# Kernel optimization log

Measured on AMD Instinct MI355X. Metric: run time of the kernel, lower is better.

The kernel has to match this reference:

```python
import jax, jax.numpy as jnp
import numpy as np

EPS = 1e-6
TEMP = 1.0
L = 64  # shapelet_len


def _znorm(a):
    # z-normalize over last axis, population std, clamped by EPS (matches torch unbiased=False + clamp_min)
    mean = a.mean(axis=-1, keepdims=True)
    std = jnp.maximum(a.std(axis=-1, keepdims=True), EPS)
    return (a - mean) / std


def setup_inputs() -> dict:
    key = jax.random.key(0)
    k1, k2 = jax.random.split(key)
    bs, T, C, P = 32, 8192, 1, 64
    x = jax.random.normal(k1, (bs, T, C), dtype=jnp.float32)
    shapelets = jax.random.normal(k2, (P, C, L), dtype=jnp.float32)
    return {"x": x, "shapelets": shapelets}


def reference(x, shapelets):
    # x: [bs, T, C]; shapelets: [P, C, L]
    bs, T, C = x.shape
    P = shapelets.shape[0]
    x_ct = jnp.transpose(x, (0, 2, 1))  # [bs, C, T]
    Tp = T - L + 1
    # sliding windows: [bs, C, T', L]
    idx = jnp.arange(Tp)[:, None] + jnp.arange(L)[None, :]
    w = x_ct[:, :, idx]
    # z-normalize windows and shapelets over the length axis
    w = _znorm(w)
    s = _znorm(shapelets)
    # squared euclidean distance via expansion ||w||^2 - 2 w.s + ||s||^2 (sum over C and L)
    w2 = jnp.sum(w * w, axis=(1, 3))          # [bs, T']
    s2 = jnp.sum(s * s, axis=(1, 2))          # [P]
    dot = jnp.einsum('bctl,pcl->btp', w, s)   # [bs, T', P]
    dist2 = w2[:, :, None] + s2[None, None, :] - 2.0 * dot
    temp = max(TEMP, EPS)
    act = jnp.exp(-dist2 / temp)              # [bs, T', P]
    # center-pad to length T: left = L//2, right = T - (T' + left)
    left = L // 2
    right = max(0, T - (Tp + left))
    act_full = jnp.pad(act, ((0, 0), (left, right), (0, 0)))
    return act_full[:, :T, :]
```

## Files before the change

### kernel.cpp

```cpp
#include <hip/hip_runtime.h>
#include <math.h>

#define T_LEN 8192
#define EPSF  1e-6f

typedef __attribute__((ext_vector_type(8))) short short8;
typedef __attribute__((ext_vector_type(4))) float float4v;

__global__ __launch_bounds__(256, 4) void shapelet_fused(
        const float* __restrict__ x,
        const float* __restrict__ sh,
        float* __restrict__ out) {
    __shared__ float Sraw[64][65];
    __shared__ unsigned short Bhi[64][72];
    __shared__ unsigned short Blo[64][72];
    __shared__ float xs[192];
    __shared__ float lmu[128], linv[128], lw2[128];
    __shared__ float lsum[64], ls2[64];

    const int tid  = threadIdx.x;
    const int lane = tid & 63;
    const int wave = tid >> 6;
    const int n    = lane & 15;
    const int quad = lane >> 4;

    const int super = blockIdx.x & 63;
    const int b     = blockIdx.x >> 6;
    const int t0    = super << 7;

    {
        const float4* g4 = (const float4*)sh;
#pragma unroll
        for (int i = 0; i < 4; ++i) {
            int idx = tid + (i << 8);
            float4 v = g4[idx];
            int e = idx << 2;
            int row = e >> 6, col = e & 63;
            Sraw[row][col + 0] = v.x;
            Sraw[row][col + 1] = v.y;
            Sraw[row][col + 2] = v.z;
            Sraw[row][col + 3] = v.w;
        }
        if (tid < 192) {
            int g = t0 - 32 + tid;
            xs[tid] = ((unsigned)g < (unsigned)T_LEN) ? x[(size_t)b * T_LEN + g] : 0.f;
        }
    }
    __syncthreads();

    if (tid < 64) {
        const int p = tid;
        float s1 = 0.f;
        for (int l = 0; l < 64; ++l) s1 += Sraw[p][l];
        float mu = s1 * (1.f / 64.f);
        float sq = 0.f;
        for (int l = 0; l < 64; ++l) { float d = Sraw[p][l] - mu; sq = fmaf(d, d, sq); }
        float sd  = fmaxf(sqrtf(sq * (1.f / 64.f)), EPSF);
        float inv = 1.f / sd;
        float ssum = 0.f, ss2 = 0.f;
        for (int l2 = 0; l2 < 32; ++l2) {
            unsigned pk_h, pk_l;
            {
                float v = Sraw[p][2 * l2];
                float s = (v - mu) * inv;
                unsigned ub = __float_as_uint(s);
                float hi = __uint_as_float(ub & 0xFFFF0000u);
                float lo = s - hi;
                unsigned lb = __float_as_uint(lo) & 0xFFFF0000u;
                pk_h = ub >> 16;
                pk_l = lb >> 16;
                float eff = hi + __uint_as_float(lb);
                ssum += eff;
                ss2  = fmaf(eff, eff, ss2);
            }
            {
                float v = Sraw[p][2 * l2 + 1];
                float s = (v - mu) * inv;
                unsigned ub = __float_as_uint(s);
                float hi = __uint_as_float(ub & 0xFFFF0000u);
                float lo = s - hi;
                unsigned lb = __float_as_uint(lo) & 0xFFFF0000u;
                pk_h |= (ub & 0xFFFF0000u);
                pk_l |= lb;
                float eff = hi + __uint_as_float(lb);
                ssum += eff;
                ss2  = fmaf(eff, eff, ss2);
            }
            *(unsigned*)&Bhi[p][2 * l2] = pk_h;
            *(unsigned*)&Blo[p][2 * l2] = pk_l;
        }
        lsum[p] = ssum;
        ls2[p]  = ss2;
    } else if (tid < 192) {
        const int r = tid - 64;
        float s1 = 0.f, sq = 0.f;
#pragma unroll
        for (int l = 0; l < 64; ++l) {
            float v = xs[r + l];
            s1 += v; sq = fmaf(v, v, sq);
        }
        float mu  = s1 * (1.f / 64.f);
        float var = fmaxf(sq * (1.f / 64.f) - mu * mu, 0.f);
        float sd  = fmaxf(sqrtf(var), EPSF);
        float inv = 1.f / sd;
        lmu[r]  = mu;
        linv[r] = inv;
        lw2[r]  = 64.f * var * inv * inv;
    }
    __syncthreads();

    short8 Bh[4][2], Bl[4][2];
#pragma unroll
    for (int pt = 0; pt < 4; ++pt)
#pragma unroll
        for (int h = 0; h < 2; ++h) {
            Bh[pt][h] = *(const short8*)&Bhi[pt * 16 + n][h * 32 + (quad << 3)];
            Bl[pt][h] = *(const short8*)&Blo[pt * 16 + n][h * 32 + (quad << 3)];
        }

#pragma unroll
    for (int u = 0; u < 2; ++u) {
        const int abase = (u << 6) + (wave << 4) + n + (quad << 3);
        short8 Ah[2], Al[2];
#pragma unroll
        for (int h = 0; h < 2; ++h) {
#pragma unroll
            for (int j = 0; j < 8; ++j) {
                float v = xs[abase + h * 32 + j];
                unsigned ub = __float_as_uint(v);
                unsigned hb = ub & 0xFFFF0000u;
                float lo = v - __uint_as_float(hb);
                Ah[h][j] = (short)(ub >> 16);
                Al[h][j] = (short)(__float_as_uint(lo) >> 16);
            }
        }

        float4v acc[4];
#pragma unroll
        for (int pt = 0; pt < 4; ++pt) {
            float4v a = {0.f, 0.f, 0.f, 0.f};
#pragma unroll
            for (int h = 0; h < 2; ++h) {
                a = __builtin_amdgcn_mfma_f32_16x16x32_bf16(Ah[h], Bh[pt][h], a, 0, 0, 0);
                a = __builtin_amdgcn_mfma_f32_16x16x32_bf16(Ah[h], Bl[pt][h], a, 0, 0, 0);
                a = __builtin_amdgcn_mfma_f32_16x16x32_bf16(Al[h], Bh[pt][h], a, 0, 0, 0);
            }
            acc[pt] = a;
        }

        float sm[4], sv[4];
#pragma unroll
        for (int pt = 0; pt < 4; ++pt) { sm[pt] = lsum[pt * 16 + n]; sv[pt] = ls2[pt * 16 + n]; }
#pragma unroll
        for (int r = 0; r < 4; ++r) {
            int tl = (u << 6) + (wave << 4) + (quad << 2) + r;
            int tg = t0 + tl;
            bool valid = (tg >= 32) && (tg <= 8160);
            float mu  = lmu[tl];
            float inv = linv[tl];
            float w2  = lw2[tl];
            float* orow = out + ((size_t)(b * T_LEN + tg) << 6);
#pragma unroll
            for (int pt = 0; pt < 4; ++pt) {
                float dot  = (acc[pt][r] - mu * sm[pt]) * inv;
                float dist = w2 + sv[pt] - 2.f * dot;
                orow[pt * 16 + n] = valid ? __expf(-dist) : 0.f;
            }
        }
    }
}

extern "C" void kernel_launch(void* const* d_in, const int* in_sizes, int n_in,
                              void* d_out, int out_size, void* d_ws, size_t ws_size,
                              hipStream_t stream) {
    const float* x  = (const float*)d_in[0];
    const float* sh = (const float*)d_in[1];
    float* out = (float*)d_out;

    shapelet_fused<<<32 * 64, 256, 0, stream>>>(x, sh, out);
}
```

Measured before the change: 85.23 us.

## Permute shapelet columns and stage outputs through LDS for float4 stores

Shapelet rows are permuted so each lane's four MFMA output columns are contiguous, which allows lsum/ls2 to be read as float4 and results packed into float4. Each wave writes its 16x64 output tile into a per-wave LDS buffer that reuses the Sraw space through a union, then reads it back and issues coalesced 16-byte global stores instead of scattered 4-byte stores. The launch-bounds occupancy hint is lowered from 4 to 3 to give the compiler more registers. The cost is extra LDS traffic per tile.

```diff
diff --git a/kernel.cpp b/kernel.cpp
--- a/kernel.cpp
+++ b/kernel.cpp
@@ -7,16 +7,20 @@
 typedef __attribute__((ext_vector_type(8))) short short8;
 typedef __attribute__((ext_vector_type(4))) float float4v;
 
-__global__ __launch_bounds__(256, 4) void shapelet_fused(
+__global__ __launch_bounds__(256, 3) void shapelet_fused(
         const float* __restrict__ x,
         const float* __restrict__ sh,
         float* __restrict__ out) {
-    __shared__ float Sraw[64][65];
+    __shared__ union {
+        float Sraw[64][65];
+        float xpose[4][1024];
+    } S;
     __shared__ unsigned short Bhi[64][72];
     __shared__ unsigned short Blo[64][72];
     __shared__ float xs[192];
     __shared__ float lmu[128], linv[128], lw2[128];
-    __shared__ float lsum[64], ls2[64];
+    __shared__ __align__(16) float lsum[64];
+    __shared__ __align__(16) float ls2[64];
 
     const int tid  = threadIdx.x;
     const int lane = tid & 63;
@@ -36,10 +40,10 @@
             float4 v = g4[idx];
             int e = idx << 2;
             int row = e >> 6, col = e & 63;
-            Sraw[row][col + 0] = v.x;
-            Sraw[row][col + 1] = v.y;
-            Sraw[row][col + 2] = v.z;
-            Sraw[row][col + 3] = v.w;
+            S.Sraw[row][col + 0] = v.x;
+            S.Sraw[row][col + 1] = v.y;
+            S.Sraw[row][col + 2] = v.z;
+            S.Sraw[row][col + 3] = v.w;
         }
         if (tid < 192) {
             int g = t0 - 32 + tid;
@@ -50,18 +54,19 @@
 
     if (tid < 64) {
         const int p = tid;
+        const int c = ((p & 3) << 4) + (p >> 2);
         float s1 = 0.f;
-        for (int l = 0; l < 64; ++l) s1 += Sraw[p][l];
+        for (int l = 0; l < 64; ++l) s1 += S.Sraw[p][l];
         float mu = s1 * (1.f / 64.f);
         float sq = 0.f;
-        for (int l = 0; l < 64; ++l) { float d = Sraw[p][l] - mu; sq = fmaf(d, d, sq); }
+        for (int l = 0; l < 64; ++l) { float d = S.Sraw[p][l] - mu; sq = fmaf(d, d, sq); }
         float sd  = fmaxf(sqrtf(sq * (1.f / 64.f)), EPSF);
         float inv = 1.f / sd;
         float ssum = 0.f, ss2 = 0.f;
         for (int l2 = 0; l2 < 32; ++l2) {
             unsigned pk_h, pk_l;
             {
-                float v = Sraw[p][2 * l2];
+                float v = S.Sraw[p][2 * l2];
                 float s = (v - mu) * inv;
                 unsigned ub = __float_as_uint(s);
                 float hi = __uint_as_float(ub & 0xFFFF0000u);
@@ -74,7 +79,7 @@
                 ss2  = fmaf(eff, eff, ss2);
             }
             {
-                float v = Sraw[p][2 * l2 + 1];
+                float v = S.Sraw[p][2 * l2 + 1];
                 float s = (v - mu) * inv;
                 unsigned ub = __float_as_uint(s);
                 float hi = __uint_as_float(ub & 0xFFFF0000u);
@@ -86,8 +91,8 @@
                 ssum += eff;
                 ss2  = fmaf(eff, eff, ss2);
             }
-            *(unsigned*)&Bhi[p][2 * l2] = pk_h;
-            *(unsigned*)&Blo[p][2 * l2] = pk_l;
+            *(unsigned*)&Bhi[c][2 * l2] = pk_h;
+            *(unsigned*)&Blo[c][2 * l2] = pk_l;
         }
         lsum[p] = ssum;
         ls2[p]  = ss2;
@@ -117,6 +122,10 @@
             Bh[pt][h] = *(const short8*)&Bhi[pt * 16 + n][h * 32 + (quad << 3)];
             Bl[pt][h] = *(const short8*)&Blo[pt * 16 + n][h * 32 + (quad << 3)];
         }
+    const float4 sm4 = *(const float4*)&lsum[n << 2];
+    const float4 sv4 = *(const float4*)&ls2[n << 2];
+
+    float* tile = S.xpose[wave];
 
 #pragma unroll
     for (int u = 0; u < 2; ++u) {
@@ -148,24 +157,34 @@
             acc[pt] = a;
         }
 
-        float sm[4], sv[4];
-#pragma unroll
-        for (int pt = 0; pt < 4; ++pt) { sm[pt] = lsum[pt * 16 + n]; sv[pt] = ls2[pt * 16 + n]; }
 #pragma unroll
         for (int r = 0; r < 4; ++r) {
-            int tl = (u << 6) + (wave << 4) + (quad << 2) + r;
+            int rloc = (quad << 2) + r;
+            int tl = (u << 6) + (wave << 4) + rloc;
             int tg = t0 + tl;
             bool valid = (tg >= 32) && (tg <= 8160);
             float mu  = lmu[tl];
             float inv = linv[tl];
             float w2  = lw2[tl];
-            float* orow = out + ((size_t)(b * T_LEN + tg) << 6);
-#pragma unroll
-            for (int pt = 0; pt < 4; ++pt) {
-                float dot  = (acc[pt][r] - mu * sm[pt]) * inv;
-                float dist = w2 + sv[pt] - 2.f * dot;
-                orow[pt * 16 + n] = valid ? __expf(-dist) : 0.f;
-            }
+            float d0 = (acc[0][r] - mu * sm4.x) * inv;
+            float d1 = (acc[1][r] - mu * sm4.y) * inv;
+            float d2 = (acc[2][r] - mu * sm4.z) * inv;
+            float d3 = (acc[3][r] - mu * sm4.w) * inv;
+            float4 o;
+            o.x = valid ? __expf(-(w2 + sv4.x - 2.f * d0)) : 0.f;
+            o.y = valid ? __expf(-(w2 + sv4.y - 2.f * d1)) : 0.f;
+            o.z = valid ? __expf(-(w2 + sv4.z - 2.f * d2)) : 0.f;
+            o.w = valid ? __expf(-(w2 + sv4.w - 2.f * d3)) : 0.f;
+            *(float4*)&tile[(rloc << 6) + (n << 2)] = o;
+        }
+
+#pragma unroll
+        for (int s = 0; s < 4; ++s) {
+            float4 v = *(const float4*)&tile[(s << 8) + (lane << 2)];
+            int rloc = (s << 2) + (lane >> 4);
+            int tg = t0 + (u << 6) + (wave << 4) + rloc;
+            int col = (lane & 15) << 2;
+            *(float4*)(out + (((size_t)(b * T_LEN + tg)) << 6) + col) = v;
         }
     }
 }
```

Result: slower. 87.37 us (+2.5%).

## Permute shapelet columns for float4 output stores and double time-tile per block

Applied to the files above, without the earlier changes.

The shapelet rows are permuted in shared memory, so each lane's four MFMA output columns (one per tile) map to four consecutive shapelets. Each lane then writes a single float4 instead of four scalar stores. The block now covers 256 time steps instead of 128, which halves the grid and spreads the per-block shapelet normalization cost over more outputs. The x window is also loaded with float4. The trade-offs are less parallelism and more shared memory per block, and the window-statistics loop is now split unevenly across threads.

```diff
diff --git a/kernel.cpp b/kernel.cpp
--- a/kernel.cpp
+++ b/kernel.cpp
@@ -14,9 +14,10 @@
     __shared__ float Sraw[64][65];
     __shared__ unsigned short Bhi[64][72];
     __shared__ unsigned short Blo[64][72];
-    __shared__ float xs[192];
-    __shared__ float lmu[128], linv[128], lw2[128];
-    __shared__ float lsum[64], ls2[64];
+    __shared__ float xs[320];
+    __shared__ float lmu[256], linv[256], lw2[256];
+    __shared__ __align__(16) float lsum[64];
+    __shared__ __align__(16) float ls2[64];
 
     const int tid  = threadIdx.x;
     const int lane = tid & 63;
@@ -24,9 +25,9 @@
     const int n    = lane & 15;
     const int quad = lane >> 4;
 
-    const int super = blockIdx.x & 63;
-    const int b     = blockIdx.x >> 6;
-    const int t0    = super << 7;
+    const int super = blockIdx.x & 31;
+    const int b     = blockIdx.x >> 5;
+    const int t0    = super << 8;
 
     {
         const float4* g4 = (const float4*)sh;
@@ -41,15 +42,27 @@
             Sraw[row][col + 2] = v.z;
             Sraw[row][col + 3] = v.w;
         }
-        if (tid < 192) {
-            int g = t0 - 32 + tid;
-            xs[tid] = ((unsigned)g < (unsigned)T_LEN) ? x[(size_t)b * T_LEN + g] : 0.f;
+        if (tid < 80) {
+            int g0 = t0 - 32 + (tid << 2);
+            float4 v;
+            if (g0 >= 0 && g0 + 3 < T_LEN) {
+                v = *(const float4*)(x + (size_t)b * T_LEN + g0);
+            } else {
+                float* vp = (float*)&v;
+#pragma unroll
+                for (int e = 0; e < 4; ++e) {
+                    int g = g0 + e;
+                    vp[e] = ((unsigned)g < (unsigned)T_LEN) ? x[(size_t)b * T_LEN + g] : 0.f;
+                }
+            }
+            *(float4*)&xs[tid << 2] = v;
         }
     }
     __syncthreads();
 
     if (tid < 64) {
         const int p = tid;
+        const int c = ((p & 3) << 4) + (p >> 2);
         float s1 = 0.f;
         for (int l = 0; l < 64; ++l) s1 += Sraw[p][l];
         float mu = s1 * (1.f / 64.f);
@@ -86,26 +99,34 @@
                 ssum += eff;
                 ss2  = fmaf(eff, eff, ss2);
             }
-            *(unsigned*)&Bhi[p][2 * l2] = pk_h;
-            *(unsigned*)&Blo[p][2 * l2] = pk_l;
+            *(unsigned*)&Bhi[c][2 * l2] = pk_h;
+            *(unsigned*)&Blo[c][2 * l2] = pk_l;
         }
         lsum[p] = ssum;
         ls2[p]  = ss2;
-    } else if (tid < 192) {
-        const int r = tid - 64;
-        float s1 = 0.f, sq = 0.f;
-#pragma unroll
-        for (int l = 0; l < 64; ++l) {
-            float v = xs[r + l];
-            s1 += v; sq = fmaf(v, v, sq);
-        }
-        float mu  = s1 * (1.f / 64.f);
-        float var = fmaxf(sq * (1.f / 64.f) - mu * mu, 0.f);
-        float sd  = fmaxf(sqrtf(var), EPSF);
-        float inv = 1.f / sd;
-        lmu[r]  = mu;
-        linv[r] = inv;
-        lw2[r]  = 64.f * var * inv * inv;
+    } else {
+        int r = tid - 64;
+#pragma unroll
+        for (int pass = 0; pass < 2; ++pass) {
+            if (pass == 0 || r < 64 + 192) {
+                float s1 = 0.f, sq = 0.f;
+#pragma unroll
+                for (int l = 0; l < 64; ++l) {
+                    float v = xs[r + l];
+                    s1 += v; sq = fmaf(v, v, sq);
+                }
+                float mu  = s1 * (1.f / 64.f);
+                float var = fmaxf(sq * (1.f / 64.f) - mu * mu, 0.f);
+                float sd  = fmaxf(sqrtf(var), EPSF);
+                float inv = 1.f / sd;
+                lmu[r]  = mu;
+                linv[r] = inv;
+                lw2[r]  = 64.f * var * inv * inv;
+            }
+            if (tid >= 128) break;
+            r = tid - 64 + 192;
+            if (pass == 1) break;
+        }
     }
     __syncthreads();
 
@@ -117,9 +138,11 @@
             Bh[pt][h] = *(const short8*)&Bhi[pt * 16 + n][h * 32 + (quad << 3)];
             Bl[pt][h] = *(const short8*)&Blo[pt * 16 + n][h * 32 + (quad << 3)];
         }
-
-#pragma unroll
-    for (int u = 0; u < 2; ++u) {
+    const float4 sm4 = *(const float4*)&lsum[n << 2];
+    const float4 sv4 = *(const float4*)&ls2[n << 2];
+
+#pragma unroll
+    for (int u = 0; u < 4; ++u) {
         const int abase = (u << 6) + (wave << 4) + n + (quad << 3);
         short8 Ah[2], Al[2];
 #pragma unroll
@@ -148,9 +171,6 @@
             acc[pt] = a;
         }
 
-        float sm[4], sv[4];
-#pragma unroll
-        for (int pt = 0; pt < 4; ++pt) { sm[pt] = lsum[pt * 16 + n]; sv[pt] = ls2[pt * 16 + n]; }
 #pragma unroll
         for (int r = 0; r < 4; ++r) {
             int tl = (u << 6) + (wave << 4) + (quad << 2) + r;
@@ -159,13 +179,16 @@
             float mu  = lmu[tl];
             float inv = linv[tl];
             float w2  = lw2[tl];
-            float* orow = out + ((size_t)(b * T_LEN + tg) << 6);
-#pragma unroll
-            for (int pt = 0; pt < 4; ++pt) {
-                float dot  = (acc[pt][r] - mu * sm[pt]) * inv;
-                float dist = w2 + sv[pt] - 2.f * dot;
-                orow[pt * 16 + n] = valid ? __expf(-dist) : 0.f;
-            }
+            float d0 = (acc[0][r] - mu * sm4.x) * inv;
+            float d1 = (acc[1][r] - mu * sm4.y) * inv;
+            float d2 = (acc[2][r] - mu * sm4.z) * inv;
+            float d3 = (acc[3][r] - mu * sm4.w) * inv;
+            float4 o;
+            o.x = valid ? __expf(-(w2 + sv4.x - 2.f * d0)) : 0.f;
+            o.y = valid ? __expf(-(w2 + sv4.y - 2.f * d1)) : 0.f;
+            o.z = valid ? __expf(-(w2 + sv4.z - 2.f * d2)) : 0.f;
+            o.w = valid ? __expf(-(w2 + sv4.w - 2.f * d3)) : 0.f;
+            *(float4*)(out + (((size_t)(b * T_LEN + tg)) << 6) + (n << 2)) = o;
         }
     }
 }
@@ -177,5 +200,5 @@
     const float* sh = (const float*)d_in[1];
     float* out = (float*)d_out;
 
-    shapelet_fused<<<32 * 64, 256, 0, stream>>>(x, sh, out);
+    shapelet_fused<<<32 * 32, 256, 0, stream>>>(x, sh, out);
 }
```

After: 82.19 us, median of 2. -3.6%, faster.
